# Kernel tuning notes

Hardware: AMD Instinct MI355X
Metric: run time of the kernel (lower is better)

The kernel has to match this reference:

```python
import jax, jax.numpy as jnp
import numpy as np

VOCAB = 12149
EMB = 50
TAGS = 9
HID = 128
START = 7
B, T = 256, 512


def setup_inputs() -> dict:
    key = jax.random.key(0)
    ks = jax.random.split(key, 12)
    s = 0.05
    return {
        "inputs": jax.random.randint(ks[0], (B, T), 0, VOCAB),
        "seq_label": jax.random.randint(ks[1], (B, T), 0, TAGS),
        "emb": jax.random.normal(ks[2], (VOCAB, EMB), jnp.float32) * s,
        "enc_Wx": jax.random.normal(ks[3], (EMB, HID), jnp.float32) * s,
        "enc_Wh": jax.random.normal(ks[4], (HID, HID), jnp.float32) * s,
        "enc_b": jnp.zeros((HID,), jnp.float32),
        "dec_emb": jax.random.normal(ks[5], (TAGS, EMB), jnp.float32) * s,
        "dec_Wx": jax.random.normal(ks[6], (EMB, HID), jnp.float32) * s,
        "dec_Wh": jax.random.normal(ks[7], (HID, HID), jnp.float32) * s,
        "dec_b": jnp.zeros((HID,), jnp.float32),
        "W": jax.random.normal(ks[8], (HID, TAGS), jnp.float32) * s,
        "b": jnp.zeros((TAGS,), jnp.float32),
    }


def _rnn(x_tbd, h0, Wx, Wh, b, collect):
    # x_tbd: [T, B, E]; SimpleRNN cell: h_t = tanh(x_t Wx + h_{t-1} Wh + b)
    def step(h, xt):
        h = jnp.tanh(xt @ Wx + h @ Wh + b)
        return h, (h if collect else None)
    hT, hs = jax.lax.scan(step, h0, x_tbd)
    return hT, hs


def reference(inputs, seq_label, emb, enc_Wx, enc_Wh, enc_b,
              dec_emb, dec_Wx, dec_Wh, dec_b, W, b):
    Bsz = inputs.shape[0]
    h0 = jnp.zeros((Bsz, HID), jnp.float32)
    # Encoder: only the final state is used as the decoder's initial state
    x = emb[inputs]                                  # [B, T, EMB]
    state, _ = _rnn(jnp.swapaxes(x, 0, 1), h0, enc_Wx, enc_Wh, enc_b, False)
    # Teacher forcing: prepend START token, drop last label
    dec_in = jnp.concatenate(
        [jnp.full((Bsz, 1), START, seq_label.dtype), seq_label], axis=1)[:, :-1]
    dx = dec_emb[dec_in]                             # [B, T, EMB]
    _, hs = _rnn(jnp.swapaxes(dx, 0, 1), state, dec_Wx, dec_Wh, dec_b, True)
    hs = jnp.swapaxes(hs, 0, 1)                      # [B, T, HID]
    return hs @ W + b                                # [B, T, TAGS]
```

## Files before the change

### kernel.cpp

```cpp
#include <hip/hip_runtime.h>
#include <hip/hip_bf16.h>

#define VOCAB 12149
#define EMB 50
#define TAGS 9
#define HID 128
#define START_TOK 7
#define BSZ 256
#define TLEN 512

typedef float v2f __attribute__((ext_vector_type(2)));
typedef _Float16 f16x2 __attribute__((ext_vector_type(2)));

__device__ __forceinline__ float tanh_fast(float x) {
  float e = __expf(2.0f * x);
  return 1.0f - 2.0f * __builtin_amdgcn_rcpf(e + 1.0f);
}

template<int CTRL>
__device__ __forceinline__ float dpp_mov(float x) {
  return __int_as_float(__builtin_amdgcn_update_dpp(
      0, __float_as_int(x), CTRL, 0xF, 0xF, true));
}
#define DPP_XOR1 0xB1

__global__ __launch_bounds__(128) void exw_kernel(
    const float* __restrict__ emb, const float* __restrict__ Wx,
    const float* __restrict__ bv, float* __restrict__ exw)
{
  __shared__ float wx_s[EMB * HID];
  __shared__ float emb_s[8 * EMB];
  const int tid = threadIdx.x;
  const int v0 = blockIdx.x * 8;
  for (int idx = tid; idx < EMB * HID; idx += 128) wx_s[idx] = Wx[idx];
  for (int idx = tid; idx < 8 * EMB; idx += 128) {
    int r = idx / EMB;
    int e = idx - r * EMB;
    int v = v0 + r;
    emb_s[idx] = (v < VOCAB) ? emb[v * EMB + e] : 0.0f;
  }
  __syncthreads();
  const float bj = bv[tid];
  for (int r = 0; r < 8; ++r) {
    int v = v0 + r;
    if (v >= VOCAB) break;
    float acc = bj;
#pragma unroll
    for (int e = 0; e < EMB; ++e) acc += emb_s[r * EMB + e] * wx_s[e * HID + tid];
    exw[v * HID + tid] = acc;
  }
}

__global__ __launch_bounds__(128, 1) void rnn_kernel(
    const int* __restrict__ inputs, const int* __restrict__ labels,
    const float* __restrict__ exw,
    const float* __restrict__ encWh,
    const float* __restrict__ dembG, const float* __restrict__ decWx,
    const float* __restrict__ decWh, const float* __restrict__ decb,
    unsigned short* __restrict__ hws16)
{
  __shared__ __align__(16) float h_s[2][HID];
  __shared__ __align__(16) float dxw_s[TAGS * HID];
  __shared__ int tok_s[TLEN];
  __shared__ int lab_s[TLEN];

  const int tid = threadIdx.x;
  const int q = tid & 1;
  const int jE = tid & ~1;
  const int bidx = blockIdx.x;

  for (int idx = tid; idx < TLEN; idx += 128) {
    tok_s[idx] = inputs[bidx * TLEN + idx];
    lab_s[idx] = labels[bidx * TLEN + idx];
  }
  for (int task = tid; task < TAGS * HID; task += 128) {
    int tag = task >> 7;
    int j2 = task & 127;
    float acc = decb[j2];
#pragma unroll
    for (int e = 0; e < EMB; ++e) acc += dembG[tag * EMB + e] * decWx[e * HID + j2];
    dxw_s[task] = acc;
  }
  h_s[0][tid] = 0.0f;

  v2f wv[64];
#pragma unroll
  for (int kk = 0; kk < 64; ++kk)
    wv[kk] = *(const v2f*)&encWh[(64 * q + kk) * HID + jE];
  __syncthreads();

  const float* exw_i = exw + tid;
  int cur = 0;

  float xv0 = exw_i[tok_s[0] * HID];
  float xv1 = exw_i[tok_s[1] * HID];
  float xv2 = exw_i[tok_s[2] * HID];
  float xv3 = exw_i[tok_s[3] * HID];

#pragma unroll 4
  for (int t = 0; t < TLEN; ++t) {
    int tn = (t + 4 < TLEN) ? t + 4 : TLEN - 1;
    float xvn = exw_i[tok_s[tn] * HID];

    const float* hb = &h_s[cur][64 * q];
    float aE0 = 0.f, aE1 = 0.f, aO0 = 0.f, aO1 = 0.f;
#pragma unroll
    for (int c = 0; c < 16; ++c) {
      float4 hv = *(const float4*)&hb[4 * c];
      aE0 += hv.x * wv[4 * c + 0].x;  aO0 += hv.x * wv[4 * c + 0].y;
      aE1 += hv.y * wv[4 * c + 1].x;  aO1 += hv.y * wv[4 * c + 1].y;
      aE0 += hv.z * wv[4 * c + 2].x;  aO0 += hv.z * wv[4 * c + 2].y;
      aE1 += hv.w * wv[4 * c + 3].x;  aO1 += hv.w * wv[4 * c + 3].y;
    }
    float aE = aE0 + aE1, aO = aO0 + aO1;
    float keep = q ? aO : aE;
    float send = q ? aE : aO;
    float v = keep + dpp_mov<DPP_XOR1>(send);
    float hn = tanh_fast(v + xv0);
    h_s[cur ^ 1][tid] = hn;
    __syncthreads();
    cur ^= 1;
    xv0 = xv1; xv1 = xv2; xv2 = xv3; xv3 = xvn;
  }

#pragma unroll
  for (int kk = 0; kk < 64; ++kk)
    wv[kk] = *(const v2f*)&decWh[(64 * q + kk) * HID + jE];

  unsigned short* hrow = hws16 + (size_t)(bidx * TLEN) * HID + tid;
  float xvD = dxw_s[START_TOK * HID + tid];
#pragma unroll 2
  for (int t = 0; t < TLEN; ++t) {
    int labn = lab_s[t];
    float xvDn = dxw_s[labn * HID + tid];

    const float* hb = &h_s[cur][64 * q];
    float aE0 = 0.f, aE1 = 0.f, aO0 = 0.f, aO1 = 0.f;
#pragma unroll
    for (int c = 0; c < 16; ++c) {
      float4 hv = *(const float4*)&hb[4 * c];
      aE0 += hv.x * wv[4 * c + 0].x;  aO0 += hv.x * wv[4 * c + 0].y;
      aE1 += hv.y * wv[4 * c + 1].x;  aO1 += hv.y * wv[4 * c + 1].y;
      aE0 += hv.z * wv[4 * c + 2].x;  aO0 += hv.z * wv[4 * c + 2].y;
      aE1 += hv.w * wv[4 * c + 3].x;  aO1 += hv.w * wv[4 * c + 3].y;
    }
    float aE = aE0 + aE1, aO = aO0 + aO1;
    float keep = q ? aO : aE;
    float send = q ? aE : aO;
    float v = keep + dpp_mov<DPP_XOR1>(send);
    float hn = tanh_fast(v + xvD);
    h_s[cur ^ 1][tid] = hn;
    hrow[(size_t)t * HID] =
        __builtin_bit_cast(unsigned short, (_Float16)hn);
    __syncthreads();
    cur ^= 1;
    xvD = xvDn;
  }
}

__global__ __launch_bounds__(256) void proj_kernel(
    const unsigned short* __restrict__ hws16, const float* __restrict__ W,
    const float* __restrict__ bout, float* __restrict__ out)
{
  __shared__ float Wt_s[TAGS][HID];
  __shared__ float bo_s[TAGS];
  const int tid = threadIdx.x;
  for (int idx = tid; idx < TAGS * HID; idx += 256) {
    int o = idx >> 7;
    int j2 = idx & 127;
    Wt_s[o][j2] = W[j2 * TAGS + o];
  }
  if (tid < TAGS) bo_s[tid] = bout[tid];
  __syncthreads();

  const int gt = blockIdx.x * 256 + tid;
  const uint2* hrow = (const uint2*)(hws16 + (size_t)gt * HID);
  float acc[TAGS];
#pragma unroll
  for (int o = 0; o < TAGS; ++o) acc[o] = bo_s[o];
#pragma unroll
  for (int c = 0; c < 32; ++c) {
    uint2 u = hrow[c];
    f16x2 p0 = __builtin_bit_cast(f16x2, u.x);
    f16x2 p1 = __builtin_bit_cast(f16x2, u.y);
    float h0 = (float)p0.x, h1 = (float)p0.y;
    float h2v = (float)p1.x, h3 = (float)p1.y;
#pragma unroll
    for (int o = 0; o < TAGS; ++o) {
      const float* wr = &Wt_s[o][4 * c];
      acc[o] += h0 * wr[0] + h1 * wr[1] + h2v * wr[2] + h3 * wr[3];
    }
  }
  float* op = &out[(size_t)gt * TAGS];
#pragma unroll
  for (int o = 0; o < TAGS; ++o) op[o] = acc[o];
}

extern "C" void kernel_launch(void* const* d_in, const int* in_sizes, int n_in,
                              void* d_out, int out_size, void* d_ws, size_t ws_size,
                              hipStream_t stream) {
  const int* inputs   = (const int*)d_in[0];
  const int* labels   = (const int*)d_in[1];
  const float* emb    = (const float*)d_in[2];
  const float* encWx  = (const float*)d_in[3];
  const float* encWh  = (const float*)d_in[4];
  const float* encb   = (const float*)d_in[5];
  const float* demb   = (const float*)d_in[6];
  const float* decWx  = (const float*)d_in[7];
  const float* decWh  = (const float*)d_in[8];
  const float* decb   = (const float*)d_in[9];
  const float* W      = (const float*)d_in[10];
  const float* bo     = (const float*)d_in[11];
  float* out = (float*)d_out;

  const size_t exw_floats = (size_t)VOCAB * HID;
  float* exw = (float*)d_ws;
  unsigned short* hws16 = (unsigned short*)((float*)d_ws + exw_floats);

  exw_kernel<<<(VOCAB + 7) / 8, 128, 0, stream>>>(emb, encWx, encb, exw);
  rnn_kernel<<<BSZ, 128, 0, stream>>>(inputs, labels, exw, encWh,
                                      demb, decWx, decWh, decb, hws16);
  proj_kernel<<<(BSZ * TLEN) / 256, 256, 0, stream>>>(hws16, W, bo, out);
}
```

Measured before the change: 372.2 us.

## Transpose decoder hidden-state storage and batch encoder gather prefetch in blocks

The decoder now packs 16 timesteps of fp16 hidden values per unit and writes them as two 16-byte stores into a [B, HID, T] layout, replacing a scattered 2-byte store on every step. The projection kernel is rewritten to one block per batch row: it stages 128-timestep tiles of the transposed hidden states in shared memory and computes the 9 tag outputs per timestep. The encoder prefetches embedding-projection rows eight steps at a time instead of through a rolling four-deep pipeline. The projection kernel keeps a leftover dummy load loop, and with only 256 blocks its parallelism may be lower than before.

```diff
diff --git a/kernel.cpp b/kernel.cpp
--- a/kernel.cpp
+++ b/kernel.cpp
@@ -92,108 +92,142 @@
   const float* exw_i = exw + tid;
   int cur = 0;
 
-  float xv0 = exw_i[tok_s[0] * HID];
-  float xv1 = exw_i[tok_s[1] * HID];
-  float xv2 = exw_i[tok_s[2] * HID];
-  float xv3 = exw_i[tok_s[3] * HID];
-
-#pragma unroll 4
-  for (int t = 0; t < TLEN; ++t) {
-    int tn = (t + 4 < TLEN) ? t + 4 : TLEN - 1;
-    float xvn = exw_i[tok_s[tn] * HID];
-
-    const float* hb = &h_s[cur][64 * q];
-    float aE0 = 0.f, aE1 = 0.f, aO0 = 0.f, aO1 = 0.f;
-#pragma unroll
-    for (int c = 0; c < 16; ++c) {
-      float4 hv = *(const float4*)&hb[4 * c];
-      aE0 += hv.x * wv[4 * c + 0].x;  aO0 += hv.x * wv[4 * c + 0].y;
-      aE1 += hv.y * wv[4 * c + 1].x;  aO1 += hv.y * wv[4 * c + 1].y;
-      aE0 += hv.z * wv[4 * c + 2].x;  aO0 += hv.z * wv[4 * c + 2].y;
-      aE1 += hv.w * wv[4 * c + 3].x;  aO1 += hv.w * wv[4 * c + 3].y;
-    }
-    float aE = aE0 + aE1, aO = aO0 + aO1;
-    float keep = q ? aO : aE;
-    float send = q ? aE : aO;
-    float v = keep + dpp_mov<DPP_XOR1>(send);
-    float hn = tanh_fast(v + xv0);
-    h_s[cur ^ 1][tid] = hn;
-    __syncthreads();
-    cur ^= 1;
-    xv0 = xv1; xv1 = xv2; xv2 = xv3; xv3 = xvn;
+  float xcur[8], xnext[8];
+#pragma unroll
+  for (int u = 0; u < 8; ++u) xcur[u] = exw_i[tok_s[u] * HID];
+
+  for (int tb = 0; tb < TLEN; tb += 8) {
+#pragma unroll
+    for (int u = 0; u < 8; ++u) {
+      int idx = tb + 8 + u;
+      if (idx > TLEN - 1) idx = TLEN - 1;
+      xnext[u] = exw_i[tok_s[idx] * HID];
+    }
+#pragma unroll
+    for (int u = 0; u < 8; ++u) {
+      const float* hb = &h_s[cur][64 * q];
+      float aE0 = 0.f, aE1 = 0.f, aO0 = 0.f, aO1 = 0.f;
+#pragma unroll
+      for (int c = 0; c < 16; ++c) {
+        float4 hv = *(const float4*)&hb[4 * c];
+        aE0 += hv.x * wv[4 * c + 0].x;  aO0 += hv.x * wv[4 * c + 0].y;
+        aE1 += hv.y * wv[4 * c + 1].x;  aO1 += hv.y * wv[4 * c + 1].y;
+        aE0 += hv.z * wv[4 * c + 2].x;  aO0 += hv.z * wv[4 * c + 2].y;
+        aE1 += hv.w * wv[4 * c + 3].x;  aO1 += hv.w * wv[4 * c + 3].y;
+      }
+      float aE = aE0 + aE1, aO = aO0 + aO1;
+      float keep = q ? aO : aE;
+      float send = q ? aE : aO;
+      float v = keep + dpp_mov<DPP_XOR1>(send);
+      float hn = tanh_fast(v + xcur[u]);
+      h_s[cur ^ 1][tid] = hn;
+      __syncthreads();
+      cur ^= 1;
+    }
+#pragma unroll
+    for (int u = 0; u < 8; ++u) xcur[u] = xnext[u];
   }
 
 #pragma unroll
   for (int kk = 0; kk < 64; ++kk)
     wv[kk] = *(const v2f*)&decWh[(64 * q + kk) * HID + jE];
 
-  unsigned short* hrow = hws16 + (size_t)(bidx * TLEN) * HID + tid;
+  unsigned int* hbase =
+      (unsigned int*)(hws16 + ((size_t)bidx * HID + tid) * TLEN);
   float xvD = dxw_s[START_TOK * HID + tid];
-#pragma unroll 2
-  for (int t = 0; t < TLEN; ++t) {
-    int labn = lab_s[t];
-    float xvDn = dxw_s[labn * HID + tid];
-
-    const float* hb = &h_s[cur][64 * q];
-    float aE0 = 0.f, aE1 = 0.f, aO0 = 0.f, aO1 = 0.f;
-#pragma unroll
-    for (int c = 0; c < 16; ++c) {
-      float4 hv = *(const float4*)&hb[4 * c];
-      aE0 += hv.x * wv[4 * c + 0].x;  aO0 += hv.x * wv[4 * c + 0].y;
-      aE1 += hv.y * wv[4 * c + 1].x;  aO1 += hv.y * wv[4 * c + 1].y;
-      aE0 += hv.z * wv[4 * c + 2].x;  aO0 += hv.z * wv[4 * c + 2].y;
-      aE1 += hv.w * wv[4 * c + 3].x;  aO1 += hv.w * wv[4 * c + 3].y;
-    }
-    float aE = aE0 + aE1, aO = aO0 + aO1;
-    float keep = q ? aO : aE;
-    float send = q ? aE : aO;
-    float v = keep + dpp_mov<DPP_XOR1>(send);
-    float hn = tanh_fast(v + xvD);
-    h_s[cur ^ 1][tid] = hn;
-    hrow[(size_t)t * HID] =
-        __builtin_bit_cast(unsigned short, (_Float16)hn);
-    __syncthreads();
-    cur ^= 1;
-    xvD = xvDn;
-  }
-}
-
-__global__ __launch_bounds__(256) void proj_kernel(
+
+  for (int tb = 0; tb < TLEN; tb += 16) {
+    unsigned int st[8];
+    unsigned int lo = 0;
+#pragma unroll
+    for (int u = 0; u < 16; ++u) {
+      const int t = tb + u;
+      int labn = lab_s[t];
+      float xvDn = dxw_s[labn * HID + tid];
+
+      const float* hb = &h_s[cur][64 * q];
+      float aE0 = 0.f, aE1 = 0.f, aO0 = 0.f, aO1 = 0.f;
+#pragma unroll
+      for (int c = 0; c < 16; ++c) {
+        float4 hv = *(const float4*)&hb[4 * c];
+        aE0 += hv.x * wv[4 * c + 0].x;  aO0 += hv.x * wv[4 * c + 0].y;
+        aE1 += hv.y * wv[4 * c + 1].x;  aO1 += hv.y * wv[4 * c + 1].y;
+        aE0 += hv.z * wv[4 * c + 2].x;  aO0 += hv.z * wv[4 * c + 2].y;
+        aE1 += hv.w * wv[4 * c + 3].x;  aO1 += hv.w * wv[4 * c + 3].y;
+      }
+      float aE = aE0 + aE1, aO = aO0 + aO1;
+      float keep = q ? aO : aE;
+      float send = q ? aE : aO;
+      float v = keep + dpp_mov<DPP_XOR1>(send);
+      float hn = tanh_fast(v + xvD);
+      h_s[cur ^ 1][tid] = hn;
+
+      unsigned int hu =
+          (unsigned int)__builtin_bit_cast(unsigned short, (_Float16)hn);
+      if ((u & 1) == 0) lo = hu;
+      else              st[u >> 1] = lo | (hu << 16);
+
+      __syncthreads();
+      cur ^= 1;
+      xvD = xvDn;
+    }
+    *(uint4*)&hbase[tb / 2]     = uint4{st[0], st[1], st[2], st[3]};
+    *(uint4*)&hbase[tb / 2 + 4] = uint4{st[4], st[5], st[6], st[7]};
+  }
+}
+
+__global__ __launch_bounds__(128) void proj_kernel(
     const unsigned short* __restrict__ hws16, const float* __restrict__ W,
     const float* __restrict__ bout, float* __restrict__ out)
 {
   __shared__ float Wt_s[TAGS][HID];
   __shared__ float bo_s[TAGS];
+  __shared__ unsigned int htile[HID][64];
+
   const int tid = threadIdx.x;
-  for (int idx = tid; idx < TAGS * HID; idx += 256) {
+  const int b = blockIdx.x;
+  for (int idx = tid; idx < TAGS * HID; idx += 128) {
     int o = idx >> 7;
     int j2 = idx & 127;
     Wt_s[o][j2] = W[j2 * TAGS + o];
   }
   if (tid < TAGS) bo_s[tid] = bout[tid];
-  __syncthreads();
-
-  const int gt = blockIdx.x * 256 + tid;
-  const uint2* hrow = (const uint2*)(hws16 + (size_t)gt * HID);
-  float acc[TAGS];
-#pragma unroll
-  for (int o = 0; o < TAGS; ++o) acc[o] = bo_s[o];
-#pragma unroll
-  for (int c = 0; c < 32; ++c) {
-    uint2 u = hrow[c];
-    f16x2 p0 = __builtin_bit_cast(f16x2, u.x);
-    f16x2 p1 = __builtin_bit_cast(f16x2, u.y);
-    float h0 = (float)p0.x, h1 = (float)p0.y;
-    float h2v = (float)p1.x, h3 = (float)p1.y;
-#pragma unroll
-    for (int o = 0; o < TAGS; ++o) {
-      const float* wr = &Wt_s[o][4 * c];
-      acc[o] += h0 * wr[0] + h1 * wr[1] + h2v * wr[2] + h3 * wr[3];
-    }
-  }
-  float* op = &out[(size_t)gt * TAGS];
-#pragma unroll
-  for (int o = 0; o < TAGS; ++o) op[o] = acc[o];
+
+  for (int tt = 0; tt < TLEN; tt += 128) {
+    __syncthreads();
+    for (int i = tid; i < HID * 16; i += 128) {
+      int j = i >> 4;
+      int p = i & 15;
+      const uint4 u = *(const uint4*)
+          (hws16 + ((size_t)b * HID + j) * TLEN + tt) + 0[&p] * 0 ;
+      (void)u;
+    }
+    for (int i = tid; i < HID * 64; i += 128) {
+      int j = i >> 6;
+      int d = i & 63;
+      htile[j][d] = *(const unsigned int*)
+          (hws16 + ((size_t)b * HID + j) * TLEN + tt + 2 * d);
+    }
+    __syncthreads();
+
+    const int t = tid;
+    float acc[TAGS];
+#pragma unroll
+    for (int o = 0; o < TAGS; ++o) acc[o] = bo_s[o];
+    const int dh = t >> 1;
+    const int hi = t & 1;
+#pragma unroll 16
+    for (int j = 0; j < HID; ++j) {
+      unsigned int u = htile[j][dh];
+      unsigned short us = hi ? (unsigned short)(u >> 16) : (unsigned short)u;
+      float hv = (float)__builtin_bit_cast(_Float16, us);
+#pragma unroll
+      for (int o = 0; o < TAGS; ++o) acc[o] += hv * Wt_s[o][j];
+    }
+    float* op = &out[((size_t)b * TLEN + tt + t) * TAGS];
+#pragma unroll
+    for (int o = 0; o < TAGS; ++o) op[o] = acc[o];
+  }
 }
 
 extern "C" void kernel_launch(void* const* d_in, const int* in_sizes, int n_in,
@@ -220,5 +254,5 @@
   exw_kernel<<<(VOCAB + 7) / 8, 128, 0, stream>>>(emb, encWx, encb, exw);
   rnn_kernel<<<BSZ, 128, 0, stream>>>(inputs, labels, exw, encWh,
                                       demb, decWx, decWh, decb, hws16);
-  proj_kernel<<<(BSZ * TLEN) / 256, 256, 0, stream>>>(hws16, W, bo, out);
-}
+  proj_kernel<<<BSZ, 128, 0, stream>>>(hws16, W, bo, out);
+}
```

Measured after the change: 464.7 us. 24.8% more time.
